# Optimization experiments

Measured on AMD Instinct MI355X. Metric: run time of the kernel, lower is better.

## Reference

```python
import jax, jax.numpy as jnp
import numpy as np
import math

BS, SEQ, DIM, H, LK = 4, 4096, 768, 12, 256
HD = DIM // H  # 64
WIN = SEQ // LK  # 16, AdaptiveAvgPool1d reduces to uniform windows since SEQ % LK == 0


def setup_inputs() -> dict:
    key = jax.random.key(0)
    ks = jax.random.split(key, 12)
    s = 1.0 / math.sqrt(DIM)
    return {
        "query": jax.random.normal(ks[0], (BS, SEQ, DIM), jnp.float32),
        "key": jax.random.normal(ks[1], (BS, SEQ, DIM), jnp.float32),
        "value": jax.random.normal(ks[2], (BS, SEQ, DIM), jnp.float32),
        "mask": jax.random.normal(ks[3], (BS, SEQ), jnp.float32),  # mask<0 -> padded
        "Wq": jax.random.normal(ks[4], (DIM, DIM), jnp.float32) * s,
        "bq": jnp.zeros((DIM,), jnp.float32),
        "Wk": jax.random.normal(ks[5], (DIM, DIM), jnp.float32) * s,
        "bk": jnp.zeros((DIM,), jnp.float32),
        "Wv": jax.random.normal(ks[6], (DIM, DIM), jnp.float32) * s,
        "bv": jnp.zeros((DIM,), jnp.float32),
        "Wo": jax.random.normal(ks[7], (DIM, DIM), jnp.float32) * s,
        "bo": jnp.zeros((DIM,), jnp.float32),
    }


def reference(query, key, value, mask, Wq, bq, Wk, bk, Wv, bv, Wo, bo):
    bs, q_len, _ = query.shape
    # projections (nn.Linear: x @ W.T + b)
    Q = query @ Wq.T + bq
    K = key @ Wk.T + bk
    V = value @ Wv.T + bv
    # mask-fill padded K/V rows with 0 (mask dim==2 path: bool_mask = mask < 0)
    keep = (mask >= 0)[:, :, None]  # [bs, seq, 1]
    K = jnp.where(keep, K, 0.0)
    V = jnp.where(keep, V, 0.0)
    # adaptive avg pool over sequence -> linformer_k=256 (uniform windows of 16)
    Kc = K.reshape(bs, LK, WIN, DIM).mean(axis=2)  # [bs, 256, dim]
    Vc = V.reshape(bs, LK, WIN, DIM).mean(axis=2)
    # split heads
    Qh = Q.reshape(bs, q_len, H, HD) / math.sqrt(HD)  # scale fused
    Kh = Kc.reshape(bs, LK, H, HD)
    Vh = Vc.reshape(bs, LK, H, HD)
    # low-rank attention: [bs, h, q_len, 256]
    scores = jnp.einsum("bqhd,bkhd->bhqk", Qh, Kh)
    weights = jax.nn.softmax(scores, axis=-1)
    context = jnp.einsum("bhqk,bkhd->bqhd", weights, Vh).reshape(bs, q_len, DIM)
    return context @ Wo.T + bo
```

## Files before the change

kernel.cpp:

```cpp
#include <hip/hip_runtime.h>

#define BS_   4
#define SEQ_  4096
#define DIM_  768
#define NH_   12
#define HD_   64
#define LK_   256

typedef __attribute__((ext_vector_type(8))) short          bf8;
typedef __attribute__((ext_vector_type(8))) unsigned short us8;
typedef __attribute__((ext_vector_type(4))) unsigned short us4;
typedef __attribute__((ext_vector_type(4))) float          f32x4;

typedef unsigned int u32g __attribute__((address_space(1)));
typedef unsigned int u32l __attribute__((address_space(3)));

#define LOG2E 1.44269504088896340736f

__device__ __forceinline__ unsigned short f2bf(float f) {
  unsigned u = __builtin_bit_cast(unsigned, f);
  u += 0x7fffu + ((u >> 16) & 1u);
  return (unsigned short)(u >> 16);
}

__device__ __forceinline__ us8 cvt8(const float* __restrict__ p) {
  const float4 a = *(const float4*)p;
  const float4 b = *(const float4*)(p + 4);
  us8 r;
  r[0] = f2bf(a.x); r[1] = f2bf(a.y); r[2] = f2bf(a.z); r[3] = f2bf(a.w);
  r[4] = f2bf(b.x); r[5] = f2bf(b.y); r[6] = f2bf(b.z); r[7] = f2bf(b.w);
  return r;
}

__device__ __forceinline__ f32x4 max4(f32x4 a, f32x4 b) {
  f32x4 r;
  r[0] = fmaxf(a[0], b[0]); r[1] = fmaxf(a[1], b[1]);
  r[2] = fmaxf(a[2], b[2]); r[3] = fmaxf(a[3], b[3]);
  return r;
}

__global__ __launch_bounds__(384) void prep_kernel(
    const float* __restrict__ key, const float* __restrict__ value,
    const float* __restrict__ mask, const float* __restrict__ query,
    const float* __restrict__ Wq, const float* __restrict__ Wk,
    const float* __restrict__ Wv, const float* __restrict__ Wo,
    unsigned short* __restrict__ pk, unsigned short* __restrict__ pv,
    float* __restrict__ frac,
    unsigned short* __restrict__ Qbf, unsigned short* __restrict__ Wbf)
{
  const int bid = blockIdx.x;
  const int tid = threadIdx.x;
  if (bid < 1024) {
    const int b = bid >> 8;
    const int l = bid & 255;
    __shared__ float keep[16];
    if (tid < 16) keep[tid] = (mask[b * SEQ_ + l * 16 + tid] >= 0.f) ? 1.f : 0.f;
    __syncthreads();
    const int isV = tid >= 192;
    const int c = isV ? tid - 192 : tid;
    const float* src = isV ? value : key;
    float4 acc = make_float4(0.f, 0.f, 0.f, 0.f);
    #pragma unroll 1
    for (int w = 0; w < 16; ++w) {
      if (keep[w] != 0.f) {
        const float4 v = *(const float4*)(src + (size_t)(b * SEQ_ + l * 16 + w) * DIM_ + c * 4);
        acc.x += v.x; acc.y += v.y; acc.z += v.z; acc.w += v.w;
      }
    }
    const float s = 1.f / 16.f;
    unsigned short* dst = isV ? pv : pk;
    us4 o4;
    o4[0] = f2bf(acc.x * s); o4[1] = f2bf(acc.y * s);
    o4[2] = f2bf(acc.z * s); o4[3] = f2bf(acc.w * s);
    *(us4*)(dst + (size_t)(b * LK_ + l) * DIM_ + c * 4) = o4;
    if (tid == 0) {
      float cnt = 0.f;
      for (int w = 0; w < 16; ++w) cnt += keep[w];
      frac[b * LK_ + l] = cnt * s;
    }
    return;
  }
  const int QN8 = (BS_ * SEQ_ * DIM_) / 8;
  const int WN8 = (DIM_ * DIM_) / 8;
  const int i = (bid - 1024) * 384 + tid;
  if (i < QN8) { *(us8*)(Qbf + (size_t)i * 8) = cvt8(query + (size_t)i * 8); return; }
  int j = i - QN8;
  const float* src; unsigned short* dst;
  if      (j <     WN8) { src = Wq; dst = Wbf;                   }
  else if (j < 2 * WN8) { src = Wk; dst = Wbf + DIM_*DIM_;     j -=     WN8; }
  else if (j < 3 * WN8) { src = Wv; dst = Wbf + 2*DIM_*DIM_;   j -= 2 * WN8; }
  else if (j < 4 * WN8) { src = Wo; dst = Wbf + 3*DIM_*DIM_;   j -= 3 * WN8; }
  else return;
  *(us8*)(dst + (size_t)j * 8) = cvt8(src + (size_t)j * 8);
}

template<int MODE, int SWZ>
__global__ __launch_bounds__(256) void gemm_bt(
    const void* __restrict__ Aptr_, const void* __restrict__ Bptr_,
    const float* __restrict__ bias, const float* __restrict__ bias2,
    const float* __restrict__ frac,
    void* __restrict__ Cout, float scale)
{
  constexpr int K  = DIM_;
  constexpr int BK = 64;
  constexpr int NT = K / BK;
  __shared__ __align__(16) unsigned short lA[128 * BK];
  __shared__ __align__(16) unsigned short lB[128 * BK];
  const int tid  = threadIdx.x;
  const int lane = tid & 63;
  const int wave = tid >> 6;

  int bx, by;
  if (SWZ) {
    const int r = (blockIdx.x & 7) * 96 + (blockIdx.x >> 3);
    bx = r / 6; by = r % 6;
  } else {
    bx = blockIdx.x; by = blockIdx.y;
  }
  const int brow = bx * 128;
  const int bcol = by * 128;

  const unsigned short* A  = (const unsigned short*)Aptr_;
  const unsigned short* Bw = (const unsigned short*)Bptr_;
  const float* bb = bias;
  int isV = 0;
  if (MODE == 34) {
    isV = blockIdx.z;
    A  += (size_t)isV * (BS_ * LK_ * DIM_);
    Bw += (size_t)isV * (DIM_ * DIM_);
    if (isV) bb = bias2;
  }

  const int wr = (wave >> 1) * 64;
  const int wc = (wave & 1) * 64;
  const int fr = lane & 15;
  const int hi = lane >> 4;
  const int rx = fr & 7;

  f32x4 acc[4][4];
  #pragma unroll
  for (int i = 0; i < 4; ++i)
    #pragma unroll
    for (int j = 0; j < 4; ++j) acc[i][j] = (f32x4){0.f, 0.f, 0.f, 0.f};

  const int srow = tid >> 3;
  const int schk = ((tid & 7) ^ (srow & 7)) * 8;

  for (int t = 0; t < NT; ++t) {
    const int k0 = t * BK;
    __syncthreads();
    #pragma unroll
    for (int s = 0; s < 4; ++s) {
      __builtin_amdgcn_global_load_lds(
          (const u32g*)(A + (size_t)(brow + srow + s * 32) * K + k0 + schk),
          (u32l*)&lA[s * 2048 + tid * 8], 16, 0, 0);
      __builtin_amdgcn_global_load_lds(
          (const u32g*)(Bw + (size_t)(bcol + srow + s * 32) * K + k0 + schk),
          (u32l*)&lB[s * 2048 + tid * 8], 16, 0, 0);
    }
    __syncthreads();
    #pragma unroll
    for (int ks = 0; ks < 2; ++ks) {
      bf8 af[4], bfv[4];
      const int c = ks * 4 + hi;
      const int pc = (c ^ rx) * 8;
      #pragma unroll
      for (int mi = 0; mi < 4; ++mi)
        af[mi] = *(const bf8*)&lA[(wr + mi * 16 + fr) * BK + pc];
      #pragma unroll
      for (int ni = 0; ni < 4; ++ni)
        bfv[ni] = *(const bf8*)&lB[(wc + ni * 16 + fr) * BK + pc];
      #pragma unroll
      for (int mi = 0; mi < 4; ++mi)
        #pragma unroll
        for (int ni = 0; ni < 4; ++ni)
          acc[mi][ni] = __builtin_amdgcn_mfma_f32_16x16x32_bf16(af[mi], bfv[ni], acc[mi][ni], 0, 0, 0);
    }
  }

  const int er = (lane >> 4) * 4;
  #pragma unroll
  for (int mi = 0; mi < 4; ++mi) {
    #pragma unroll
    for (int ni = 0; ni < 4; ++ni) {
      #pragma unroll
      for (int j = 0; j < 4; ++j) {
        const int r = brow + wr + mi * 16 + er + j;
        const int c = bcol + wc + ni * 16 + fr;
        float v = acc[mi][ni][j];
        if (MODE == 0) {
          v = (v + bias[c]) * scale;
          ((unsigned short*)Cout)[(size_t)r * DIM_ + c] = f2bf(v);
        } else if (MODE == 2) {
          ((float*)Cout)[(size_t)r * DIM_ + c] = v + bias[c];
        } else {
          v += frac[r] * bb[c];
          const int bb_ = r >> 8, key = r & 255;
          const int hh = c >> 6, dd = c & 63;
          const int bh = bb_ * NH_ + hh;
          size_t idx;
          if (isV) {
            idx = (size_t)bh * 16384 +
                ((key >> 5) * 4 + (dd >> 4)) * 512 + ((key >> 3) & 3) * 128 +
                (dd & 15) * 8 + (key & 7) + 786432;
          } else {
            const int tt = key >> 5, g = (key >> 3) & 3, sub = (key >> 2) & 1, jj = key & 3;
            const int frk = g * 4 + jj;
            idx = (size_t)bh * 16384 +
                (((tt * 2 + sub) * 2) + (dd >> 5)) * 512 + ((dd >> 3) & 3) * 128 +
                frk * 8 + (dd & 7);
          }
          ((unsigned short*)Cout)[idx] = f2bf(v);
        }
      }
    }
  }
}

__global__ __launch_bounds__(512, 4) void attn_fused(
    const unsigned short* __restrict__ Qh,
    const unsigned short* __restrict__ Kf,
    const unsigned short* __restrict__ Vf,
    unsigned short* __restrict__ ctx)
{
  __shared__ __align__(16) unsigned short Ks[16384];
  const int tid  = threadIdx.x;
  const int lane = tid & 63;
  const int wave = tid >> 6;
  const int bh = blockIdx.y;
  const int b = bh / NH_, h = bh % NH_;
  const int fr = lane & 15;
  const int hi = lane >> 4;
  const int qrow = blockIdx.x * 128 + wave * 16;

  {
    const unsigned short* kg = Kf + (size_t)bh * 16384 + tid * 8;
    #pragma unroll
    for (int i = 0; i < 4; ++i)
      __builtin_amdgcn_global_load_lds((const u32g*)(kg + i * 4096),
                                       (u32l*)&Ks[i * 4096 + tid * 8], 16, 0, 0);
  }

  const unsigned short* qp = Qh + (size_t)(b * SEQ_ + qrow + fr) * DIM_ + h * HD_ + hi * 8;
  const bf8 q0 = *(const bf8*)qp;
  const bf8 q1 = *(const bf8*)(qp + 32);

  __syncthreads();

  f32x4 scA[8], scB[8];
  __builtin_amdgcn_s_setprio(1);
  #pragma unroll
  for (int s = 0; s < 8; ++s) {
    const bf8 ka0 = *(const bf8*)&Ks[(s * 4 + 0) * 512 + lane * 8];
    const bf8 ka1 = *(const bf8*)&Ks[(s * 4 + 1) * 512 + lane * 8];
    const bf8 kb0 = *(const bf8*)&Ks[(s * 4 + 2) * 512 + lane * 8];
    const bf8 kb1 = *(const bf8*)&Ks[(s * 4 + 3) * 512 + lane * 8];
    f32x4 x = (f32x4){0.f, 0.f, 0.f, 0.f};
    x = __builtin_amdgcn_mfma_f32_16x16x32_bf16(ka0, q0, x, 0, 0, 0);
    x = __builtin_amdgcn_mfma_f32_16x16x32_bf16(ka1, q1, x, 0, 0, 0);
    scA[s] = x;
    f32x4 y = (f32x4){0.f, 0.f, 0.f, 0.f};
    y = __builtin_amdgcn_mfma_f32_16x16x32_bf16(kb0, q0, y, 0, 0, 0);
    y = __builtin_amdgcn_mfma_f32_16x16x32_bf16(kb1, q1, y, 0, 0, 0);
    scB[s] = y;
  }
  __builtin_amdgcn_s_setprio(0);

  f32x4 tm[8];
  #pragma unroll
  for (int s = 0; s < 8; ++s) tm[s] = max4(scA[s], scB[s]);
  tm[0] = max4(tm[0], tm[4]); tm[1] = max4(tm[1], tm[5]);
  tm[2] = max4(tm[2], tm[6]); tm[3] = max4(tm[3], tm[7]);
  tm[0] = max4(tm[0], tm[2]); tm[1] = max4(tm[1], tm[3]);
  tm[0] = max4(tm[0], tm[1]);
  float m = fmaxf(fmaxf(tm[0][0], tm[0][1]), fmaxf(tm[0][2], tm[0][3]));
  m = fmaxf(m, __shfl_xor(m, 16));
  m = fmaxf(m, __shfl_xor(m, 32));

  f32x4 uA = (f32x4){0.f, 0.f, 0.f, 0.f};
  f32x4 uB = (f32x4){0.f, 0.f, 0.f, 0.f};
  #pragma unroll
  for (int s = 0; s < 8; ++s) {
    #pragma unroll
    for (int j = 0; j < 4; ++j) {
      scA[s][j] = exp2f(scA[s][j] - m);
      scB[s][j] = exp2f(scB[s][j] - m);
    }
    uA += scA[s];
    uB += scB[s];
  }
  const f32x4 uv = uA + uB;
  float sum = (uv[0] + uv[1]) + (uv[2] + uv[3]);
  sum += __shfl_xor(sum, 16);
  sum += __shfl_xor(sum, 32);
  const float inv = 1.f / sum;

  bf8 pa[8];
  #pragma unroll
  for (int s = 0; s < 8; ++s) {
    bf8 p;
    #pragma unroll
    for (int j = 0; j < 4; ++j) {
      p[j]     = (short)f2bf(scA[s][j] * inv);
      p[4 + j] = (short)f2bf(scB[s][j] * inv);
    }
    pa[s] = p;
  }

  const unsigned short* vb = Vf + (size_t)bh * 16384 + lane * 8;
  f32x4 acc[4];
  #pragma unroll
  for (int ct = 0; ct < 4; ++ct) acc[ct] = (f32x4){0.f, 0.f, 0.f, 0.f};
  __builtin_amdgcn_s_setprio(1);
  #pragma unroll
  for (int s = 0; s < 8; ++s) {
    #pragma unroll
    for (int ct = 0; ct < 4; ++ct) {
      const bf8 vf = *(const bf8*)(vb + (s * 4 + ct) * 512);
      acc[ct] = __builtin_amdgcn_mfma_f32_16x16x32_bf16(pa[s], vf, acc[ct], 0, 0, 0);
    }
  }
  __builtin_amdgcn_s_setprio(0);

  #pragma unroll
  for (int ct = 0; ct < 4; ++ct)
    #pragma unroll
    for (int j = 0; j < 4; ++j)
      ctx[(size_t)(b * SEQ_ + qrow + hi * 4 + j) * DIM_ + h * HD_ + ct * 16 + fr] =
          f2bf(acc[ct][j]);
}

extern "C" void kernel_launch(void* const* d_in, const int* in_sizes, int n_in,
                              void* d_out, int out_size, void* d_ws, size_t ws_size,
                              hipStream_t stream) {
  const float* query = (const float*)d_in[0];
  const float* key   = (const float*)d_in[1];
  const float* value = (const float*)d_in[2];
  const float* mask  = (const float*)d_in[3];
  const float* Wq    = (const float*)d_in[4];
  const float* bq    = (const float*)d_in[5];
  const float* Wk    = (const float*)d_in[6];
  const float* bk    = (const float*)d_in[7];
  const float* Wv    = (const float*)d_in[8];
  const float* bv    = (const float*)d_in[9];
  const float* Wo    = (const float*)d_in[10];
  const float* bo    = (const float*)d_in[11];
  float* out = (float*)d_out;

  char* ws = (char*)d_ws;
  unsigned short* Qh  = (unsigned short*)ws;
  unsigned short* ctx = (unsigned short*)(ws + 25165824);
  unsigned short* pK  = (unsigned short*)(ws + 50331648);
  unsigned short* pV  = (unsigned short*)(ws + 51904512);
  unsigned short* Kf  = (unsigned short*)(ws + 53477376);
  unsigned short* Vf  = (unsigned short*)(ws + 55050240);
  float*          frac = (float*)(ws + 56623104);
  unsigned short* Wbf = (unsigned short*)(ws + 56627200);
  unsigned short* Qbf = ctx;

  const float qscale = 0.125f * LOG2E;

  prep_kernel<<<dim3(5888), dim3(384), 0, stream>>>(
      key, value, mask, query, Wq, Wk, Wv, Wo, pK, pV, frac, Qbf, Wbf);
  gemm_bt<0, 1><<<dim3(768), dim3(256), 0, stream>>>(
      Qbf, Wbf, bq, nullptr, nullptr, Qh, qscale);
  gemm_bt<34, 0><<<dim3(8, 6, 2), dim3(256), 0, stream>>>(
      pK, Wbf + DIM_*DIM_, bk, bv, frac, Kf, 1.f);
  attn_fused<<<dim3(32, 48), dim3(512), 0, stream>>>(Qh, Kf, Vf, ctx);
  gemm_bt<2, 1><<<dim3(768), dim3(256), 0, stream>>>(
      ctx, Wbf + 3*DIM_*DIM_, bo, nullptr, nullptr, out, 1.f);
}
```

Baseline: 135.1 us.

## Double-buffer LDS tiles in projection GEMM with async global-to-LDS prefetch

Splits the GEMM shared-memory tiles into two buffers and issues the global_load_lds for tile t+2 while tile t is being computed, using vmcnt waits and raw barriers instead of two __syncthreads per iteration. This aims to hide global memory latency behind MFMA work. It doubles LDS use per block (64KB), which may lower occupancy, and relies on hand-counted vmcnt values being correct.

Result: faster. 129.8 us (-3.9%).

```diff
diff --git a/kernel.cpp b/kernel.cpp
--- a/kernel.cpp
+++ b/kernel.cpp
@@ -104,8 +104,8 @@
   constexpr int K  = DIM_;
   constexpr int BK = 64;
   constexpr int NT = K / BK;
-  __shared__ __align__(16) unsigned short lA[128 * BK];
-  __shared__ __align__(16) unsigned short lB[128 * BK];
+  __shared__ __align__(16) unsigned short lA[2][128 * BK];
+  __shared__ __align__(16) unsigned short lB[2][128 * BK];
   const int tid  = threadIdx.x;
   const int lane = tid & 63;
   const int wave = tid >> 6;
@@ -146,19 +146,20 @@
   const int srow = tid >> 3;
   const int schk = ((tid & 7) ^ (srow & 7)) * 8;
 
-  for (int t = 0; t < NT; ++t) {
+  auto STAGE = [&](int t, int b) {
     const int k0 = t * BK;
-    __syncthreads();
     #pragma unroll
     for (int s = 0; s < 4; ++s) {
       __builtin_amdgcn_global_load_lds(
           (const u32g*)(A + (size_t)(brow + srow + s * 32) * K + k0 + schk),
-          (u32l*)&lA[s * 2048 + tid * 8], 16, 0, 0);
+          (u32l*)&lA[b][s * 2048 + tid * 8], 16, 0, 0);
       __builtin_amdgcn_global_load_lds(
           (const u32g*)(Bw + (size_t)(bcol + srow + s * 32) * K + k0 + schk),
-          (u32l*)&lB[s * 2048 + tid * 8], 16, 0, 0);
-    }
-    __syncthreads();
+          (u32l*)&lB[b][s * 2048 + tid * 8], 16, 0, 0);
+    }
+  };
+
+  auto COMPUTE = [&](int b) {
     #pragma unroll
     for (int ks = 0; ks < 2; ++ks) {
       bf8 af[4], bfv[4];
@@ -166,15 +167,35 @@
       const int pc = (c ^ rx) * 8;
       #pragma unroll
       for (int mi = 0; mi < 4; ++mi)
-        af[mi] = *(const bf8*)&lA[(wr + mi * 16 + fr) * BK + pc];
+        af[mi] = *(const bf8*)&lA[b][(wr + mi * 16 + fr) * BK + pc];
       #pragma unroll
       for (int ni = 0; ni < 4; ++ni)
-        bfv[ni] = *(const bf8*)&lB[(wc + ni * 16 + fr) * BK + pc];
+        bfv[ni] = *(const bf8*)&lB[b][(wc + ni * 16 + fr) * BK + pc];
       #pragma unroll
       for (int mi = 0; mi < 4; ++mi)
         #pragma unroll
         for (int ni = 0; ni < 4; ++ni)
           acc[mi][ni] = __builtin_amdgcn_mfma_f32_16x16x32_bf16(af[mi], bfv[ni], acc[mi][ni], 0, 0, 0);
+    }
+  };
+
+  STAGE(0, 0);
+  STAGE(1, 1);
+  asm volatile("s_waitcnt vmcnt(8)" ::: "memory");
+  __builtin_amdgcn_s_barrier();
+
+  #pragma unroll 2
+  for (int t = 0; t < NT; ++t) {
+    COMPUTE(t & 1);
+    if (t + 1 < NT) {
+      __builtin_amdgcn_s_barrier();
+      if (t + 2 < NT) {
+        STAGE(t + 2, t & 1);
+        asm volatile("s_waitcnt vmcnt(8)" ::: "memory");
+      } else {
+        asm volatile("s_waitcnt vmcnt(0)" ::: "memory");
+      }
+      __builtin_amdgcn_s_barrier();
     }
   }
 
```
